# Performance work log

Measured on AMD Instinct MI355X. Metric: run time of the kernel, lower is better.

The kernel has to match this reference:

```python
import jax, jax.numpy as jnp
import numpy as np

D_MODEL = 1024
N_HEADS = 16
D_HEAD = D_MODEL // N_HEADS
D_FF = 4096
EPS = 1e-6  # flax LayerNorm default


def setup_inputs() -> dict:
    key = jax.random.key(0)
    ks = jax.random.split(key, 16)
    s = 1.0 / np.sqrt(D_MODEL)
    inp = {
        'x':  jax.random.normal(ks[0], (4, 2048, D_MODEL), jnp.float32),
        'Wq': jax.random.normal(ks[1], (D_MODEL, D_MODEL), jnp.float32) * s,
        'bq': jnp.zeros((D_MODEL,), jnp.float32),
        'Wk': jax.random.normal(ks[2], (D_MODEL, D_MODEL), jnp.float32) * s,
        'bk': jnp.zeros((D_MODEL,), jnp.float32),
        'Wv': jax.random.normal(ks[3], (D_MODEL, D_MODEL), jnp.float32) * s,
        'bv': jnp.zeros((D_MODEL,), jnp.float32),
        'Wo': jax.random.normal(ks[4], (D_MODEL, D_MODEL), jnp.float32) * s,
        'W1': jax.random.normal(ks[5], (D_MODEL, D_FF), jnp.float32) * s,
        'b1': jnp.zeros((D_FF,), jnp.float32),
        'W2': jax.random.normal(ks[6], (D_FF, D_MODEL), jnp.float32) * (1.0 / np.sqrt(D_FF)),
        'b2': jnp.zeros((D_MODEL,), jnp.float32),
        'g1': jnp.ones((D_MODEL,), jnp.float32),
        'beta1': jnp.zeros((D_MODEL,), jnp.float32),
        'g2': jnp.ones((D_MODEL,), jnp.float32),
        'beta2': jnp.zeros((D_MODEL,), jnp.float32),
    }
    return inp


def _layernorm(x, g, b):
    mu = jnp.mean(x, axis=-1, keepdims=True)
    var = jnp.mean(jnp.square(x - mu), axis=-1, keepdims=True)
    return (x - mu) * jax.lax.rsqrt(var + EPS) * g + b


def _attention(x, Wq, bq, Wk, bk, Wv, bv, Wo):
    B, S, D = x.shape
    def split_heads(t):
        return t.reshape(B, S, N_HEADS, D_HEAD).transpose(0, 2, 1, 3)  # bhsd
    q = split_heads(x @ Wq + bq)
    k = split_heads(x @ Wk + bk)
    v = split_heads(x @ Wv + bv)
    scale = jnp.sqrt(jnp.float32(D_HEAD))
    scores = jnp.einsum('bhsd,bhtd->bhst', q, k) / scale
    causal = jnp.tril(jnp.ones((S, S), dtype=jnp.bool_))
    scores = jnp.where(causal, scores, jnp.finfo(scores.dtype).min)
    w = jax.nn.softmax(scores, axis=-1)
    out = jnp.einsum('bhst,bhtd->bhsd', w, v)
    out = out.transpose(0, 2, 1, 3).reshape(B, S, D)
    return out @ Wo  # o_proj has no bias


def reference(x, Wq, bq, Wk, bk, Wv, bv, Wo, W1, b1, W2, b2, g1, beta1, g2, beta2):
    normed = _layernorm(x, g1, beta1)
    x = x + _attention(normed, Wq, bq, Wk, bk, Wv, bv, Wo)
    normed = _layernorm(x, g2, beta2)
    h = jax.nn.gelu(normed @ W1 + b1)  # approximate tanh gelu, matching flax nn.gelu
    x = x + (h @ W2 + b2)
    return x
```

## Files before the change

kernel.cpp:

```cpp
#include <hip/hip_runtime.h>

#define SEQ 2048
#define NROWS 8192
#define NH 16
#define DHEAD 64
#define QLD 3072

typedef float f32x4 __attribute__((ext_vector_type(4)));
typedef __bf16 bf16x8 __attribute__((ext_vector_type(8)));

__device__ __forceinline__ unsigned short f2bf(float f) {
  union { float f; unsigned u; } v; v.f = f;
  unsigned r = v.u + 0x7fffu + ((v.u >> 16) & 1u);
  return (unsigned short)(r >> 16);
}

__device__ __forceinline__ void gl16(const void* g, void* l) {
  __builtin_amdgcn_global_load_lds((const __attribute__((address_space(1))) void*)g,
                                   (__attribute__((address_space(3))) void*)l, 16, 0, 0);
}

__device__ __forceinline__ float gelu_f(float x) {
  float t = 0.7978845608028654f * (x + 0.044715f * x * x * x);
  float e = __expf(2.0f * t);
  float th = 1.0f - 2.0f / (e + 1.0f);
  return 0.5f * x * (1.0f + th);
}

#define CVTPK(dst, lo, hi) asm("v_cvt_pk_bf16_f32 %0, %1, %2" : "=v"(dst) : "v"(lo), "v"(hi))

#if __has_builtin(__builtin_amdgcn_permlane32_swap)
#define P32SWAP(a, b, x, y) { auto _t = __builtin_amdgcn_permlane32_swap((a), (b), false, false); (x) = _t[0]; (y) = _t[1]; }
#else
#define P32SWAP(a, b, x, y) { unsigned _as = (unsigned)__shfl_xor((int)(a), 32, 64); \
  unsigned _bs = (unsigned)__shfl_xor((int)(b), 32, 64); \
  (x) = (l < 32) ? (a) : _bs; (y) = (l < 32) ? _as : (b); }
#endif
#if __has_builtin(__builtin_amdgcn_permlane16_swap)
#define P16SWAP(a, b, x, y) { auto _t = __builtin_amdgcn_permlane16_swap((a), (b), false, false); (x) = _t[0]; (y) = _t[1]; }
#else
#define P16SWAP(a, b, x, y) { unsigned _as = (unsigned)__shfl_xor((int)(a), 16, 64); \
  unsigned _bs = (unsigned)__shfl_xor((int)(b), 16, 64); \
  (x) = (l & 16) ? _bs : (a); (y) = (l & 16) ? (b) : _as; }
#endif

#define MEMFENCE asm volatile("" ::: "memory")
#define BAR() do { MEMFENCE; __builtin_amdgcn_s_barrier(); MEMFENCE; } while (0)
#define WAIT_LGKM0 asm volatile("s_waitcnt lgkmcnt(0)" ::: "memory")
#define WAIT_VM6 asm volatile("s_waitcnt vmcnt(6)" ::: "memory")
#define WAIT_VM0 asm volatile("s_waitcnt vmcnt(0)" ::: "memory")

__global__ __launch_bounds__(256) void transpose_cvt(const float* __restrict__ W,
                                                     unsigned short* __restrict__ Wt,
                                                     int K, int N) {
  __shared__ float tile[32][33];
  const int tx = threadIdx.x, ty = threadIdx.y;
  const int n0 = blockIdx.x * 32, k0 = blockIdx.y * 32;
#pragma unroll
  for (int i = ty; i < 32; i += 8)
    tile[i][tx] = W[(size_t)(k0 + i) * N + n0 + tx];
  __syncthreads();
#pragma unroll
  for (int i = ty; i < 32; i += 8)
    Wt[(size_t)(n0 + i) * K + k0 + tx] = f2bf(tile[tx][i]);
}

__global__ __launch_bounds__(256) void concat_bias(const float* __restrict__ bq,
                                                   const float* __restrict__ bk,
                                                   const float* __restrict__ bv,
                                                   float* __restrict__ dst) {
  int i = blockIdx.x * 256 + threadIdx.x;
  if (i < 1024) dst[i] = bq[i];
  else if (i < 2048) dst[i] = bk[i - 1024];
  else if (i < 3072) dst[i] = bv[i - 2048];
}

__global__ __launch_bounds__(256) void layernorm_k(const float* __restrict__ x,
                                                   const float* __restrict__ g,
                                                   const float* __restrict__ b,
                                                   unsigned short* __restrict__ out) {
  const int row = blockIdx.x, tid = threadIdx.x;
  const float4 v = reinterpret_cast<const float4*>(x + (size_t)row * 1024)[tid];
  float s = v.x + v.y + v.z + v.w;
  float s2 = v.x * v.x + v.y * v.y + v.z * v.z + v.w * v.w;
#pragma unroll
  for (int d = 1; d < 64; d <<= 1) { s += __shfl_xor(s, d, 64); s2 += __shfl_xor(s2, d, 64); }
  __shared__ float ls[4], ls2[4];
  const int w = tid >> 6;
  if ((tid & 63) == 0) { ls[w] = s; ls2[w] = s2; }
  __syncthreads();
  s = ls[0] + ls[1] + ls[2] + ls[3];
  s2 = ls2[0] + ls2[1] + ls2[2] + ls2[3];
  const float mu = s * (1.0f / 1024.0f);
  const float var = s2 * (1.0f / 1024.0f) - mu * mu;
  const float rstd = rsqrtf(var + 1e-6f);
  const float4 gv = reinterpret_cast<const float4*>(g)[tid];
  const float4 bv = reinterpret_cast<const float4*>(b)[tid];
  ushort4 o;
  o.x = f2bf((v.x - mu) * rstd * gv.x + bv.x);
  o.y = f2bf((v.y - mu) * rstd * gv.y + bv.y);
  o.z = f2bf((v.z - mu) * rstd * gv.z + bv.z);
  o.w = f2bf((v.w - mu) * rstd * gv.w + bv.w);
  reinterpret_cast<ushort4*>(out + (size_t)row * 1024)[tid] = o;
}

enum { EP_BIAS = 1, EP_RES = 2, EP_GELU = 4, EP_BF16 = 8, EP_QSCALE = 16 };

template <int E>
__global__ __launch_bounds__(512) void gemm3_k(const unsigned short* __restrict__ A,
                                               const unsigned short* __restrict__ Bt,
                                               const float* __restrict__ bias,
                                               const float* __restrict__ resid,
                                               void* __restrict__ out,
                                               int M, int N, int K) {
  __shared__ __align__(16) unsigned short Ls[3][24576];
  const int tid = threadIdx.x;
  const int l = tid & 63, w = tid >> 6;
  const int lr = l & 15, lg = l >> 4;
  const int wr = w >> 1, wc = w & 1;

  const int gx = gridDim.x;
  const int nwg = gx * gridDim.y;
  int lin = blockIdx.y * gx + blockIdx.x;
  lin = (lin & 7) * (nwg >> 3) + (lin >> 3);
  const int bn = lin % gx, bm = lin / gx;

  const unsigned short* Ab = A + (size_t)(bm * 256) * K;
  const unsigned short* Bb = Bt + (size_t)(bn * 128) * K;
  const int NK = K >> 6;

  const int srow8 = l >> 3;
  const int sslot = (l & 7) ^ srow8;
  const size_t rs8 = (size_t)8 * K * 2;

  auto stage = [&](int slot, int t) {
    if (t >= NK) return;
    char* base = (char*)(&Ls[slot][0]);
    const char* a0 = (const char*)(Ab + (size_t)srow8 * K + t * 64) + sslot * 16;
    const char* b0 = (const char*)(Bb + (size_t)srow8 * K + t * 64) + sslot * 16;
    gl16(a0 + (size_t)w * rs8,        base + w * 1024 + l * 16);
    gl16(a0 + (size_t)(8 + w) * rs8,  base + (8 + w) * 1024 + l * 16);
    gl16(a0 + (size_t)(16 + w) * rs8, base + (16 + w) * 1024 + l * 16);
    gl16(a0 + (size_t)(24 + w) * rs8, base + (24 + w) * 1024 + l * 16);
    gl16(b0 + (size_t)w * rs8,        base + 32768 + w * 1024 + l * 16);
    gl16(b0 + (size_t)(8 + w) * rs8,  base + 32768 + (8 + w) * 1024 + l * 16);
  };
  auto rd = [&](const char* base, int r, int ks) {
    return *reinterpret_cast<const bf16x8*>(base + r * 128 + (((ks << 2) + lg) ^ (r & 7)) * 16);
  };

  f32x4 acc[4][4];
#pragma unroll
  for (int m = 0; m < 4; ++m)
#pragma unroll
    for (int n = 0; n < 4; ++n) acc[m][n] = 0.0f;

  stage(0, 0);
  stage(1, 1);
  int cs = 0, ss = 2;

  for (int t = 0; t < NK; ++t) {
    if (t + 1 < NK) { WAIT_VM6; } else { WAIT_VM0; }
    BAR();
    stage(ss, t + 2);

    const char* Ac = (const char*)(&Ls[cs][0]);
    const char* Bc = Ac + 32768;
    bf16x8 af[4][2], bf[4][2];
#pragma unroll
    for (int mi = 0; mi < 4; ++mi)
#pragma unroll
      for (int ks = 0; ks < 2; ++ks) af[mi][ks] = rd(Ac, wr * 64 + mi * 16 + lr, ks);
#pragma unroll
    for (int ni = 0; ni < 4; ++ni)
#pragma unroll
      for (int ks = 0; ks < 2; ++ks) bf[ni][ks] = rd(Bc, wc * 64 + ni * 16 + lr, ks);

    __builtin_amdgcn_s_setprio(1);
#pragma unroll
    for (int mi = 0; mi < 4; ++mi)
#pragma unroll
      for (int ni = 0; ni < 4; ++ni)
#pragma unroll
        for (int ks = 0; ks < 2; ++ks)
          acc[mi][ni] = __builtin_amdgcn_mfma_f32_16x16x32_bf16(af[mi][ks], bf[ni][ks], acc[mi][ni], 0, 0, 0);
    __builtin_amdgcn_s_setprio(0);
    WAIT_LGKM0;

    cs = (cs == 2) ? 0 : cs + 1;
    ss = (ss == 2) ? 0 : ss + 1;
  }

  const int row0 = bm * 256 + wr * 64;
  const int col0 = bn * 128 + wc * 64;
#pragma unroll
  for (int m = 0; m < 4; ++m) {
#pragma unroll
    for (int n = 0; n < 4; ++n) {
      const int col = col0 + n * 16 + lr;
      float bc = 0.0f;
      if (E & EP_BIAS) bc = bias[col];
#pragma unroll
      for (int j = 0; j < 4; ++j) {
        const int row = row0 + m * 16 + lg * 4 + j;
        float v = acc[m][n][j] + bc;
        if (E & EP_RES) v += resid[(size_t)row * N + col];
        if (E & EP_GELU) v = gelu_f(v);
        if (E & EP_QSCALE) { if (col < 1024) v *= 0.18033688011112042f; }
        if (E & EP_BF16) ((unsigned short*)out)[(size_t)row * N + col] = f2bf(v);
        else ((float*)out)[(size_t)row * N + col] = v;
      }
    }
  }
}

__global__ __launch_bounds__(512, 2) void attn_k(const unsigned short* __restrict__ qkv,
                                                 unsigned short* __restrict__ out) {
  __shared__ __align__(16) unsigned short Kl[2][128 * 64];
  __shared__ __align__(16) unsigned short Vt[2][64 * 128];
  const int tid = threadIdx.x;
  const int l = tid & 63, w = tid >> 6;
  const int lr = l & 15, lg = l >> 4;
  const int bh = blockIdx.y;
  const int b = bh >> 4, h = bh & 15;
  const size_t rowbase = (size_t)b * SEQ;
  char* klb = (char*)Kl;
  char* vtb = (char*)Vt;

  const int srow8 = l >> 3;
  const int kslot = (l & 7) ^ (srow8 & 7);
  auto stageK = [&](int buf, int kb2) {
#pragma unroll
    for (int s = w; s < 16; s += 8) {
      const char* src = (const char*)(qkv + (rowbase + kb2 + s * 8 + srow8) * QLD + 1024 + h * 64)
                        + kslot * 16;
      gl16(src, klb + buf * 16384 + s * 1024 + l * 16);
    }
  };
  const int sg = tid & 31, dhg = tid >> 5;
  auto loadV = [&](int kb2, uint2* vr) {
#pragma unroll
    for (int i = 0; i < 4; ++i)
      vr[i] = *reinterpret_cast<const uint2*>(
          qkv + (rowbase + kb2 + sg * 4 + i) * QLD + 2048 + h * 64 + dhg * 4);
  };
  auto writeV = [&](int buf, const uint2* vr) {
    char* vb = vtb + buf * 16384;
#pragma unroll
    for (int jj = 0; jj < 4; ++jj) {
      const int dh = dhg * 4 + jj;
      unsigned a0 = (jj < 2) ? vr[0].x : vr[0].y;
      unsigned a1 = (jj < 2) ? vr[1].x : vr[1].y;
      unsigned a2 = (jj < 2) ? vr[2].x : vr[2].y;
      unsigned a3 = (jj < 2) ? vr[3].x : vr[3].y;
      unsigned s01, s23;
      if (jj & 1) {
        s01 = (a0 >> 16) | (a1 & 0xffff0000u);
        s23 = (a2 >> 16) | (a3 & 0xffff0000u);
      } else {
        s01 = (a0 & 0xffffu) | (a1 << 16);
        s23 = (a2 & 0xffffu) | (a3 << 16);
      }
      const int bo = dh * 256 + (((sg >> 1) ^ (dh & 15)) << 4) + ((sg & 1) << 3);
      uint2 p; p.x = s01; p.y = s23;
      *reinterpret_cast<uint2*>(vb + bo) = p;
    }
  };

#pragma unroll 1
  for (int seg = 0; seg < 2; ++seg) {
    const int qt = seg ? (15 - blockIdx.x) : blockIdx.x;
    const int q0 = qt << 7;
    const int qwmin = q0 + w * 16;
    const int qrow = qwmin + lr;

    bf16x8 qf[2];
#pragma unroll
    for (int ks = 0; ks < 2; ++ks)
      qf[ks] = *reinterpret_cast<const bf16x8*>(
          qkv + (rowbase + qrow) * QLD + h * 64 + ks * 32 + lg * 8);

    f32x4 oacc[4];
#pragma unroll
    for (int n = 0; n < 4; ++n) oacc[n] = 0.0f;
    float mrun = -1e30f, lrun = 0.0f;

    {
      stageK(0, 0);
      uint2 vr0[4];
      loadV(0, vr0);
      writeV(0, vr0);
    }
    __syncthreads();

#pragma unroll 1
    for (int kt = 0; kt <= qt; ++kt) {
      const int cur = kt & 1, nb = cur ^ 1;
      const int kb = kt << 7;
      const bool more = kt < qt;
      uint2 vr[4];
      if (more) { stageK(nb, kb + 128); loadV(kb + 128, vr); }

      f32x4 sacc[8];
#pragma unroll
      for (int ni = 0; ni < 8; ++ni) sacc[ni] = 0.0f;
      const char* kc = klb + cur * 16384;
      __builtin_amdgcn_s_setprio(1);
#pragma unroll
      for (int ks = 0; ks < 2; ++ks) {
#pragma unroll
        for (int ni = 0; ni < 8; ++ni) {
          const int r = ni * 16 + lr;
          const int bo = r * 128 + ((((ks << 2) + lg) ^ (r & 7)) << 4);
          bf16x8 kf = *reinterpret_cast<const bf16x8*>(kc + bo);
          sacc[ni] = __builtin_amdgcn_mfma_f32_16x16x32_bf16(kf, qf[ks], sacc[ni], 0, 0, 0);
        }
      }
      __builtin_amdgcn_s_setprio(0);

      if (kt == qt) {
#pragma unroll
        for (int ni = 0; ni < 8; ++ni)
#pragma unroll
          for (int j = 0; j < 4; ++j)
            if (kb + ni * 16 + lg * 4 + j > qrow) sacc[ni][j] = -1e30f;
      }

      float pm = sacc[0][0];
#pragma unroll
      for (int ni = 0; ni < 8; ++ni)
#pragma unroll
        for (int j = 0; j < 4; ++j) pm = fmaxf(pm, sacc[ni][j]);
      pm = fmaxf(pm, __shfl_xor(pm, 16, 64));
      pm = fmaxf(pm, __shfl_xor(pm, 32, 64));
      if (!__all(pm <= mrun + 8.0f)) {
        const float mnew = fmaxf(mrun, pm);
        const float alpha = exp2f(mrun - mnew);
        mrun = mnew;
        lrun *= alpha;
#pragma unroll
        for (int n = 0; n < 4; ++n) oacc[n] *= alpha;
      }
      float rs = 0.0f;
#pragma unroll
      for (int ni = 0; ni < 8; ++ni)
#pragma unroll
        for (int j = 0; j < 4; ++j) {
          const float p = exp2f(sacc[ni][j] - mrun);
          sacc[ni][j] = p;
          rs += p;
        }
      rs += __shfl_xor(rs, 16, 64);
      rs += __shfl_xor(rs, 32, 64);
      lrun += rs;

      if (more) writeV(nb, vr);

      const char* vc = vtb + cur * 16384;
#pragma unroll
      for (int g = 0; g < 4; ++g) {
        unsigned U0, U1, U2, U3, C0, C1, W0, W1, W2, W3;
        CVTPK(U0, sacc[2 * g][0], sacc[2 * g][1]);
        CVTPK(U1, sacc[2 * g][2], sacc[2 * g][3]);
        CVTPK(U2, sacc[2 * g + 1][0], sacc[2 * g + 1][1]);
        CVTPK(U3, sacc[2 * g + 1][2], sacc[2 * g + 1][3]);
        P32SWAP(U0, U2, C0, C1);
        P16SWAP(C0, C1, W0, W2);
        P32SWAP(U1, U3, C0, C1);
        P16SWAP(C0, C1, W1, W3);
        union { uint4 u; bf16x8 v; } pu;
        pu.u = make_uint4(W0, W1, W2, W3);
        __builtin_amdgcn_s_setprio(1);
#pragma unroll
        for (int n = 0; n < 4; ++n) {
          const int r = n * 16 + lr;
          const int bo = r * 256 + ((((g << 2) + lg) ^ (r & 15)) << 4);
          bf16x8 vf = *reinterpret_cast<const bf16x8*>(vc + bo);
          oacc[n] = __builtin_amdgcn_mfma_f32_16x16x32_bf16(vf, pu.v, oacc[n], 0, 0, 0);
        }
        __builtin_amdgcn_s_setprio(0);
      }
      __syncthreads();
    }

    const float inv = 1.0f / lrun;
#pragma unroll
    for (int n = 0; n < 4; ++n) {
      ushort4 o;
      o.x = f2bf(oacc[n][0] * inv);
      o.y = f2bf(oacc[n][1] * inv);
      o.z = f2bf(oacc[n][2] * inv);
      o.w = f2bf(oacc[n][3] * inv);
      *reinterpret_cast<ushort4*>(out + (rowbase + qrow) * 1024 + h * 64 + n * 16 + lg * 4) = o;
    }
  }
}

extern "C" void kernel_launch(void* const* d_in, const int* in_sizes, int n_in,
                              void* d_out, int out_size, void* d_ws, size_t ws_size,
                              hipStream_t stream) {
  const float* x   = (const float*)d_in[0];
  const float* Wq  = (const float*)d_in[1];
  const float* bq  = (const float*)d_in[2];
  const float* Wk  = (const float*)d_in[3];
  const float* bk  = (const float*)d_in[4];
  const float* Wv  = (const float*)d_in[5];
  const float* bv  = (const float*)d_in[6];
  const float* Wo  = (const float*)d_in[7];
  const float* W1  = (const float*)d_in[8];
  const float* b1  = (const float*)d_in[9];
  const float* W2  = (const float*)d_in[10];
  const float* b2  = (const float*)d_in[11];
  const float* g1  = (const float*)d_in[12];
  const float* be1 = (const float*)d_in[13];
  const float* g2  = (const float*)d_in[14];
  const float* be2 = (const float*)d_in[15];

  char* ws = (char*)d_ws;
  size_t off = 0;
  auto alloc = [&](size_t bytes) { char* p = ws + off; off += (bytes + 255) & ~(size_t)255; return p; };
  unsigned short* WqkvT = (unsigned short*)alloc((size_t)3072 * 1024 * 2);
  unsigned short* WoT   = (unsigned short*)alloc((size_t)1024 * 1024 * 2);
  unsigned short* W1T   = (unsigned short*)alloc((size_t)4096 * 1024 * 2);
  unsigned short* W2T   = (unsigned short*)alloc((size_t)1024 * 4096 * 2);
  float*          bqkv  = (float*)alloc((size_t)3072 * 4);
  unsigned short* normed = (unsigned short*)alloc((size_t)NROWS * 1024 * 2);
  unsigned short* qkvbuf = (unsigned short*)alloc((size_t)NROWS * 4096 * 2);
  unsigned short* attnb  = (unsigned short*)alloc((size_t)NROWS * 1024 * 2);
  float*          x1     = (float*)alloc((size_t)NROWS * 1024 * 4);

  const dim3 tb(32, 8);
  transpose_cvt<<<dim3(32, 32), tb, 0, stream>>>(Wq, WqkvT, 1024, 1024);
  transpose_cvt<<<dim3(32, 32), tb, 0, stream>>>(Wk, WqkvT + 1024 * 1024, 1024, 1024);
  transpose_cvt<<<dim3(32, 32), tb, 0, stream>>>(Wv, WqkvT + 2 * 1024 * 1024, 1024, 1024);
  transpose_cvt<<<dim3(32, 32), tb, 0, stream>>>(Wo, WoT, 1024, 1024);
  transpose_cvt<<<dim3(128, 32), tb, 0, stream>>>(W1, W1T, 1024, 4096);
  transpose_cvt<<<dim3(32, 128), tb, 0, stream>>>(W2, W2T, 4096, 1024);
  concat_bias<<<12, 256, 0, stream>>>(bq, bk, bv, bqkv);

  layernorm_k<<<NROWS, 256, 0, stream>>>(x, g1, be1, normed);
  gemm3_k<(EP_BIAS | EP_BF16 | EP_QSCALE)><<<dim3(24, 32), 512, 0, stream>>>(normed, WqkvT, bqkv, nullptr, qkvbuf, NROWS, 3072, 1024);
  attn_k<<<dim3(8, 64), 512, 0, stream>>>(qkvbuf, attnb);
  gemm3_k<EP_RES><<<dim3(8, 32), 512, 0, stream>>>(attnb, WoT, nullptr, x, x1, NROWS, 1024, 1024);
  layernorm_k<<<NROWS, 256, 0, stream>>>(x1, g2, be2, normed);
  gemm3_k<(EP_BIAS | EP_GELU | EP_BF16)><<<dim3(32, 32), 512, 0, stream>>>(normed, W1T, b1, nullptr, qkvbuf, NROWS, 4096, 1024);
  gemm3_k<(EP_BIAS | EP_RES)><<<dim3(8, 32), 512, 0, stream>>>(qkvbuf, W2T, b2, x1, d_out, NROWS, 1024, 4096);
}
```

Measured before the change: 542.2 us.

## Add 256x256 double-buffered GEMM for QKV/FFN1 and shrink attention key tiles to 64

Adds a new gemm2_k using 256x256 output tiles with a two-stage LDS pipeline, used for the QKV projection and the first FFN GEMM, to raise arithmetic intensity per block. The attention kernel now processes 64-key tiles with half-size LDS buffers and an occupancy hint of 4. It also skips fully masked key tiles per wave to cut wasted causal work. The trade-off is a larger accumulator footprint (one block per CU) in the GEMM, and more loop iterations and barriers in attention.

```diff
diff --git a/kernel.cpp b/kernel.cpp
--- a/kernel.cpp
+++ b/kernel.cpp
@@ -47,6 +47,7 @@
 #define MEMFENCE asm volatile("" ::: "memory")
 #define BAR() do { MEMFENCE; __builtin_amdgcn_s_barrier(); MEMFENCE; } while (0)
 #define WAIT_LGKM0 asm volatile("s_waitcnt lgkmcnt(0)" ::: "memory")
+#define WAIT_VM8 asm volatile("s_waitcnt vmcnt(8)" ::: "memory")
 #define WAIT_VM6 asm volatile("s_waitcnt vmcnt(6)" ::: "memory")
 #define WAIT_VM0 asm volatile("s_waitcnt vmcnt(0)" ::: "memory")
 
@@ -107,6 +108,119 @@
 enum { EP_BIAS = 1, EP_RES = 2, EP_GELU = 4, EP_BF16 = 8, EP_QSCALE = 16 };
 
 template <int E>
+__global__ __launch_bounds__(512, 1) void gemm2_k(const unsigned short* __restrict__ A,
+                                                  const unsigned short* __restrict__ Bt,
+                                                  const float* __restrict__ bias,
+                                                  const float* __restrict__ resid,
+                                                  void* __restrict__ out,
+                                                  int M, int N, int K) {
+  __shared__ __align__(16) unsigned short Ls[2][32768];
+  const int tid = threadIdx.x;
+  const int l = tid & 63, w = tid >> 6;
+  const int lr = l & 15, lg = l >> 4;
+  const int wr = w >> 2, wc = w & 3;
+
+  const int gx = gridDim.x;
+  const int nwg = gx * gridDim.y;
+  int lin = blockIdx.y * gx + blockIdx.x;
+  lin = (lin & 7) * (nwg >> 3) + (lin >> 3);
+  const int bn = lin % gx, bm = lin / gx;
+
+  const unsigned short* Ab = A + (size_t)(bm * 256) * K;
+  const unsigned short* Bb = Bt + (size_t)(bn * 256) * K;
+  const int NK = K >> 6;
+
+  const int srow8 = l >> 3;
+  const int sslot = (l & 7) ^ srow8;
+
+  auto stage = [&](int slot, int t) {
+    char* base = (char*)(&Ls[slot][0]);
+    const char* a0 = (const char*)(Ab + (size_t)srow8 * K + t * 64) + sslot * 16;
+    const char* b0 = (const char*)(Bb + (size_t)srow8 * K + t * 64) + sslot * 16;
+    const size_t rs8 = (size_t)8 * K * 2;
+#pragma unroll
+    for (int i = 0; i < 4; ++i)
+      gl16(a0 + (size_t)(8 * i + w) * rs8, base + (8 * i + w) * 1024 + l * 16);
+#pragma unroll
+    for (int i = 0; i < 4; ++i)
+      gl16(b0 + (size_t)(8 * i + w) * rs8, base + 32768 + (8 * i + w) * 1024 + l * 16);
+  };
+  auto rd = [&](const char* base, int r, int ks) {
+    return *reinterpret_cast<const bf16x8*>(base + r * 128 + (((ks << 2) + lg) ^ (r & 7)) * 16);
+  };
+
+  f32x4 acc[8][4];
+#pragma unroll
+  for (int m = 0; m < 8; ++m)
+#pragma unroll
+    for (int n = 0; n < 4; ++n) acc[m][n] = 0.0f;
+
+  stage(0, 0);
+
+  for (int t = 0; t < NK; ++t) {
+    const int cs = t & 1, nb = cs ^ 1;
+    if (t + 1 < NK) { stage(nb, t + 1); WAIT_VM8; } else { WAIT_VM0; }
+    BAR();
+
+    const char* Ac = (const char*)(&Ls[cs][0]);
+    const char* Bc = Ac + 32768;
+    bf16x8 bf[4][2], a0[4][2], a1[4][2];
+#pragma unroll
+    for (int ni = 0; ni < 4; ++ni)
+#pragma unroll
+      for (int ks = 0; ks < 2; ++ks) bf[ni][ks] = rd(Bc, wc * 64 + ni * 16 + lr, ks);
+#pragma unroll
+    for (int mi = 0; mi < 4; ++mi)
+#pragma unroll
+      for (int ks = 0; ks < 2; ++ks) a0[mi][ks] = rd(Ac, wr * 128 + mi * 16 + lr, ks);
+#pragma unroll
+    for (int mi = 0; mi < 4; ++mi)
+#pragma unroll
+      for (int ks = 0; ks < 2; ++ks) a1[mi][ks] = rd(Ac, wr * 128 + (4 + mi) * 16 + lr, ks);
+
+    __builtin_amdgcn_s_setprio(1);
+#pragma unroll
+    for (int mi = 0; mi < 4; ++mi)
+#pragma unroll
+      for (int ni = 0; ni < 4; ++ni)
+#pragma unroll
+        for (int ks = 0; ks < 2; ++ks)
+          acc[mi][ni] = __builtin_amdgcn_mfma_f32_16x16x32_bf16(a0[mi][ks], bf[ni][ks], acc[mi][ni], 0, 0, 0);
+#pragma unroll
+    for (int mi = 0; mi < 4; ++mi)
+#pragma unroll
+      for (int ni = 0; ni < 4; ++ni)
+#pragma unroll
+        for (int ks = 0; ks < 2; ++ks)
+          acc[4 + mi][ni] = __builtin_amdgcn_mfma_f32_16x16x32_bf16(a1[mi][ks], bf[ni][ks], acc[4 + mi][ni], 0, 0, 0);
+    __builtin_amdgcn_s_setprio(0);
+    BAR();
+  }
+
+  const int row0 = bm * 256 + wr * 128;
+  const int col0 = bn * 256 + wc * 64;
+#pragma unroll
+  for (int m = 0; m < 8; ++m) {
+#pragma unroll
+    for (int n = 0; n < 4; ++n) {
+      const int col = col0 + n * 16 + lr;
+      float bc = 0.0f;
+      if (E & EP_BIAS) bc = bias[col];
+#pragma unroll
+      for (int j = 0; j < 4; ++j) {
+        const int row = row0 + m * 16 + lg * 4 + j;
+        float v = acc[m][n][j] + bc;
+        if (E & EP_RES) v += resid[(size_t)row * N + col];
+        if (E & EP_GELU) v = gelu_f(v);
+        if (E & EP_QSCALE) { if (col < 1024) v *= 0.18033688011112042f; }
+        if (E & EP_BF16) ((unsigned short*)out)[(size_t)row * N + col] = f2bf(v);
+        else ((float*)out)[(size_t)row * N + col] = v;
+      }
+    }
+  }
+}
+
+template <int E>
 __global__ __launch_bounds__(512) void gemm3_k(const unsigned short* __restrict__ A,
                                                const unsigned short* __restrict__ Bt,
                                                const float* __restrict__ bias,
@@ -214,10 +328,10 @@
   }
 }
 
-__global__ __launch_bounds__(512, 2) void attn_k(const unsigned short* __restrict__ qkv,
+__global__ __launch_bounds__(512, 4) void attn_k(const unsigned short* __restrict__ qkv,
                                                  unsigned short* __restrict__ out) {
-  __shared__ __align__(16) unsigned short Kl[2][128 * 64];
-  __shared__ __align__(16) unsigned short Vt[2][64 * 128];
+  __shared__ __align__(16) unsigned short Kl[2][4096];
+  __shared__ __align__(16) unsigned short Vt[2][4096];
   const int tid = threadIdx.x;
   const int l = tid & 63, w = tid >> 6;
   const int lr = l & 15, lg = l >> 4;
@@ -226,44 +340,44 @@
   const size_t rowbase = (size_t)b * SEQ;
   char* klb = (char*)Kl;
   char* vtb = (char*)Vt;
-
-  const int srow8 = l >> 3;
-  const int kslot = (l & 7) ^ (srow8 & 7);
+  const int sg = tid & 15, dhg = tid >> 4;
+
   auto stageK = [&](int buf, int kb2) {
-#pragma unroll
-    for (int s = w; s < 16; s += 8) {
-      const char* src = (const char*)(qkv + (rowbase + kb2 + s * 8 + srow8) * QLD + 1024 + h * 64)
-                        + kslot * 16;
-      gl16(src, klb + buf * 16384 + s * 1024 + l * 16);
-    }
-  };
-  const int sg = tid & 31, dhg = tid >> 5;
+    const int r = (w << 3) + (l >> 3);
+    const char* src = (const char*)(qkv + (rowbase + kb2 + r) * QLD + 1024 + h * 64)
+                      + 16 * ((l & 7) ^ (l >> 3));
+    gl16(src, klb + buf * 8192 + (w << 10) + (l << 4));
+  };
   auto loadV = [&](int kb2, uint2* vr) {
-#pragma unroll
-    for (int i = 0; i < 4; ++i)
-      vr[i] = *reinterpret_cast<const uint2*>(
-          qkv + (rowbase + kb2 + sg * 4 + i) * QLD + 2048 + h * 64 + dhg * 4);
+    if (tid < 256) {
+#pragma unroll
+      for (int i = 0; i < 4; ++i)
+        vr[i] = *reinterpret_cast<const uint2*>(
+            qkv + (rowbase + kb2 + sg * 4 + i) * QLD + 2048 + h * 64 + dhg * 4);
+    }
   };
   auto writeV = [&](int buf, const uint2* vr) {
-    char* vb = vtb + buf * 16384;
-#pragma unroll
-    for (int jj = 0; jj < 4; ++jj) {
-      const int dh = dhg * 4 + jj;
-      unsigned a0 = (jj < 2) ? vr[0].x : vr[0].y;
-      unsigned a1 = (jj < 2) ? vr[1].x : vr[1].y;
-      unsigned a2 = (jj < 2) ? vr[2].x : vr[2].y;
-      unsigned a3 = (jj < 2) ? vr[3].x : vr[3].y;
-      unsigned s01, s23;
-      if (jj & 1) {
-        s01 = (a0 >> 16) | (a1 & 0xffff0000u);
-        s23 = (a2 >> 16) | (a3 & 0xffff0000u);
-      } else {
-        s01 = (a0 & 0xffffu) | (a1 << 16);
-        s23 = (a2 & 0xffffu) | (a3 << 16);
+    if (tid < 256) {
+      char* vb = vtb + buf * 8192;
+#pragma unroll
+      for (int jj = 0; jj < 4; ++jj) {
+        const int dh = dhg * 4 + jj;
+        unsigned a0 = (jj < 2) ? vr[0].x : vr[0].y;
+        unsigned a1 = (jj < 2) ? vr[1].x : vr[1].y;
+        unsigned a2 = (jj < 2) ? vr[2].x : vr[2].y;
+        unsigned a3 = (jj < 2) ? vr[3].x : vr[3].y;
+        unsigned s01, s23;
+        if (jj & 1) {
+          s01 = (a0 >> 16) | (a1 & 0xffff0000u);
+          s23 = (a2 >> 16) | (a3 & 0xffff0000u);
+        } else {
+          s01 = (a0 & 0xffffu) | (a1 << 16);
+          s23 = (a2 & 0xffffu) | (a3 << 16);
+        }
+        const int bo = (dh * 128 + sg * 8) ^ ((dh & 7) << 4);
+        uint2 p; p.x = s01; p.y = s23;
+        *reinterpret_cast<uint2*>(vb + bo) = p;
       }
-      const int bo = dh * 256 + (((sg >> 1) ^ (dh & 15)) << 4) + ((sg & 1) << 3);
-      uint2 p; p.x = s01; p.y = s23;
-      *reinterpret_cast<uint2*>(vb + bo) = p;
     }
   };
 
@@ -271,6 +385,7 @@
   for (int seg = 0; seg < 2; ++seg) {
     const int qt = seg ? (15 - blockIdx.x) : blockIdx.x;
     const int q0 = qt << 7;
+    const int ktmax = 2 * qt + 1;
     const int qwmin = q0 + w * 16;
     const int qrow = qwmin + lr;
 
@@ -294,91 +409,96 @@
     __syncthreads();
 
 #pragma unroll 1
-    for (int kt = 0; kt <= qt; ++kt) {
+    for (int kt = 0; kt <= ktmax; ++kt) {
       const int cur = kt & 1, nb = cur ^ 1;
-      const int kb = kt << 7;
-      const bool more = kt < qt;
+      const int kb = kt << 6;
+      const bool more = kt < ktmax;
+      const bool active = kb <= qwmin + 15;
       uint2 vr[4];
-      if (more) { stageK(nb, kb + 128); loadV(kb + 128, vr); }
-
-      f32x4 sacc[8];
-#pragma unroll
-      for (int ni = 0; ni < 8; ++ni) sacc[ni] = 0.0f;
-      const char* kc = klb + cur * 16384;
-      __builtin_amdgcn_s_setprio(1);
-#pragma unroll
-      for (int ks = 0; ks < 2; ++ks) {
-#pragma unroll
-        for (int ni = 0; ni < 8; ++ni) {
-          const int r = ni * 16 + lr;
-          const int bo = r * 128 + ((((ks << 2) + lg) ^ (r & 7)) << 4);
-          bf16x8 kf = *reinterpret_cast<const bf16x8*>(kc + bo);
-          sacc[ni] = __builtin_amdgcn_mfma_f32_16x16x32_bf16(kf, qf[ks], sacc[ni], 0, 0, 0);
-        }
-      }
-      __builtin_amdgcn_s_setprio(0);
-
-      if (kt == qt) {
-#pragma unroll
-        for (int ni = 0; ni < 8; ++ni)
-#pragma unroll
-          for (int j = 0; j < 4; ++j)
-            if (kb + ni * 16 + lg * 4 + j > qrow) sacc[ni][j] = -1e30f;
-      }
-
-      float pm = sacc[0][0];
-#pragma unroll
-      for (int ni = 0; ni < 8; ++ni)
-#pragma unroll
-        for (int j = 0; j < 4; ++j) pm = fmaxf(pm, sacc[ni][j]);
-      pm = fmaxf(pm, __shfl_xor(pm, 16, 64));
-      pm = fmaxf(pm, __shfl_xor(pm, 32, 64));
-      if (!__all(pm <= mrun + 8.0f)) {
-        const float mnew = fmaxf(mrun, pm);
-        const float alpha = exp2f(mrun - mnew);
-        mrun = mnew;
-        lrun *= alpha;
-#pragma unroll
-        for (int n = 0; n < 4; ++n) oacc[n] *= alpha;
-      }
-      float rs = 0.0f;
-#pragma unroll
-      for (int ni = 0; ni < 8; ++ni)
-#pragma unroll
-        for (int j = 0; j < 4; ++j) {
-          const float p = exp2f(sacc[ni][j] - mrun);
-          sacc[ni][j] = p;
-          rs += p;
-        }
-      rs += __shfl_xor(rs, 16, 64);
-      rs += __shfl_xor(rs, 32, 64);
-      lrun += rs;
-
-      if (more) writeV(nb, vr);
-
-      const char* vc = vtb + cur * 16384;
-#pragma unroll
-      for (int g = 0; g < 4; ++g) {
-        unsigned U0, U1, U2, U3, C0, C1, W0, W1, W2, W3;
-        CVTPK(U0, sacc[2 * g][0], sacc[2 * g][1]);
-        CVTPK(U1, sacc[2 * g][2], sacc[2 * g][3]);
-        CVTPK(U2, sacc[2 * g + 1][0], sacc[2 * g + 1][1]);
-        CVTPK(U3, sacc[2 * g + 1][2], sacc[2 * g + 1][3]);
-        P32SWAP(U0, U2, C0, C1);
-        P16SWAP(C0, C1, W0, W2);
-        P32SWAP(U1, U3, C0, C1);
-        P16SWAP(C0, C1, W1, W3);
-        union { uint4 u; bf16x8 v; } pu;
-        pu.u = make_uint4(W0, W1, W2, W3);
+      if (more) { stageK(nb, (kt + 1) << 6); loadV((kt + 1) << 6, vr); }
+
+      f32x4 sacc[4];
+      if (active) {
+#pragma unroll
+        for (int ni = 0; ni < 4; ++ni) sacc[ni] = 0.0f;
+        const char* kc = klb + cur * 8192;
         __builtin_amdgcn_s_setprio(1);
 #pragma unroll
-        for (int n = 0; n < 4; ++n) {
-          const int r = n * 16 + lr;
-          const int bo = r * 256 + ((((g << 2) + lg) ^ (r & 15)) << 4);
-          bf16x8 vf = *reinterpret_cast<const bf16x8*>(vc + bo);
-          oacc[n] = __builtin_amdgcn_mfma_f32_16x16x32_bf16(vf, pu.v, oacc[n], 0, 0, 0);
+        for (int ks = 0; ks < 2; ++ks) {
+#pragma unroll
+          for (int ni = 0; ni < 4; ++ni) {
+            const int r = ni * 16 + lr;
+            const int bo = (r * 128 + ks * 64 + lg * 16) ^ ((lr & 7) << 4);
+            bf16x8 kf = *reinterpret_cast<const bf16x8*>(kc + bo);
+            sacc[ni] = __builtin_amdgcn_mfma_f32_16x16x32_bf16(kf, qf[ks], sacc[ni], 0, 0, 0);
+          }
         }
         __builtin_amdgcn_s_setprio(0);
+
+        if (kb + 63 > qwmin) {
+#pragma unroll
+          for (int ni = 0; ni < 4; ++ni)
+#pragma unroll
+            for (int j = 0; j < 4; ++j)
+              if (kb + ni * 16 + lg * 4 + j > qrow) sacc[ni][j] = -1e30f;
+        }
+
+        float pm = sacc[0][0];
+#pragma unroll
+        for (int ni = 0; ni < 4; ++ni)
+#pragma unroll
+          for (int j = 0; j < 4; ++j) pm = fmaxf(pm, sacc[ni][j]);
+        pm = fmaxf(pm, __shfl_xor(pm, 16, 64));
+        pm = fmaxf(pm, __shfl_xor(pm, 32, 64));
+        if (!__all(pm <= mrun + 8.0f)) {
+          const float mnew = fmaxf(mrun, pm);
+          const float alpha = exp2f(mrun - mnew);
+          mrun = mnew;
+          lrun *= alpha;
+#pragma unroll
+          for (int n = 0; n < 4; ++n) oacc[n] *= alpha;
+        }
+        float rs = 0.0f;
+#pragma unroll
+        for (int ni = 0; ni < 4; ++ni)
+#pragma unroll
+          for (int j = 0; j < 4; ++j) {
+            const float p = exp2f(sacc[ni][j] - mrun);
+            sacc[ni][j] = p;
+            rs += p;
+          }
+        rs += __shfl_xor(rs, 16, 64);
+        rs += __shfl_xor(rs, 32, 64);
+        lrun += rs;
+      }
+
+      if (more) writeV(nb, vr);
+
+      if (active) {
+        const char* vc = vtb + cur * 8192;
+#pragma unroll
+        for (int ks2 = 0; ks2 < 2; ++ks2) {
+          unsigned U0, U1, U2, U3, C0, C1, W0, W1, W2, W3;
+          CVTPK(U0, sacc[2 * ks2][0], sacc[2 * ks2][1]);
+          CVTPK(U1, sacc[2 * ks2][2], sacc[2 * ks2][3]);
+          CVTPK(U2, sacc[2 * ks2 + 1][0], sacc[2 * ks2 + 1][1]);
+          CVTPK(U3, sacc[2 * ks2 + 1][2], sacc[2 * ks2 + 1][3]);
+          P32SWAP(U0, U2, C0, C1);
+          P16SWAP(C0, C1, W0, W2);
+          P32SWAP(U1, U3, C0, C1);
+          P16SWAP(C0, C1, W1, W3);
+          union { uint4 u; bf16x8 v; } pu;
+          pu.u = make_uint4(W0, W1, W2, W3);
+          __builtin_amdgcn_s_setprio(1);
+#pragma unroll
+          for (int n = 0; n < 4; ++n) {
+            const int r = n * 16 + lr;
+            const int bo = (r * 128 + ks2 * 64 + lg * 16) ^ ((lr & 7) << 4);
+            bf16x8 vf = *reinterpret_cast<const bf16x8*>(vc + bo);
+            oacc[n] = __builtin_amdgcn_mfma_f32_16x16x32_bf16(vf, pu.v, oacc[n], 0, 0, 0);
+          }
+          __builtin_amdgcn_s_setprio(0);
+        }
       }
       __syncthreads();
     }
@@ -439,10 +559,10 @@
   concat_bias<<<12, 256, 0, stream>>>(bq, bk, bv, bqkv);
 
   layernorm_k<<<NROWS, 256, 0, stream>>>(x, g1, be1, normed);
-  gemm3_k<(EP_BIAS | EP_BF16 | EP_QSCALE)><<<dim3(24, 32), 512, 0, stream>>>(normed, WqkvT, bqkv, nullptr, qkvbuf, NROWS, 3072, 1024);
+  gemm2_k<(EP_BIAS | EP_BF16 | EP_QSCALE)><<<dim3(12, 32), 512, 0, stream>>>(normed, WqkvT, bqkv, nullptr, qkvbuf, NROWS, 3072, 1024);
   attn_k<<<dim3(8, 64), 512, 0, stream>>>(qkvbuf, attnb);
   gemm3_k<EP_RES><<<dim3(8, 32), 512, 0, stream>>>(attnb, WoT, nullptr, x, x1, NROWS, 1024, 1024);
   layernorm_k<<<NROWS, 256, 0, stream>>>(x1, g2, be2, normed);
-  gemm3_k<(EP_BIAS | EP_GELU | EP_BF16)><<<dim3(32, 32), 512, 0, stream>>>(normed, W1T, b1, nullptr, qkvbuf, NROWS, 4096, 1024);
+  gemm2_k<(EP_BIAS | EP_GELU | EP_BF16)><<<dim3(16, 32), 512, 0, stream>>>(normed, W1T, b1, nullptr, qkvbuf, NROWS, 4096, 1024);
   gemm3_k<(EP_BIAS | EP_RES)><<<dim3(8, 32), 512, 0, stream>>>(qkvbuf, W2T, b2, x1, d_out, NROWS, 1024, 4096);
 }
```

Result: faster. 523.1 us (-3.5%).
